# Kernel tuning notes

Measured on AMD Instinct MI355X. Metric: run time of the kernel, lower is better.

Reference implementation:

```python
import jax, jax.numpy as jnp
import numpy as np

B, CIN, N, E = 8192, 16, 96, 768
NF, EMB, NCLS = 64, 128, 210


def _p(key, shape, scale=0.05):
    return jax.random.normal(key, shape, dtype=jnp.float32) * scale


def setup_inputs() -> dict:
    key = jax.random.key(0)
    ks = jax.random.split(key, 20)
    return {
        "src": jax.random.normal(ks[0], (B, CIN, N), dtype=jnp.float32),
        "edge_index": jax.random.randint(ks[1], (2, E), 0, N, dtype=jnp.int32),
        "gcn1_w": _p(ks[2], (CIN, 64)), "gcn1_b": _p(ks[3], (64,)),
        "gcn2_w": _p(ks[4], (64, 32)), "gcn2_b": _p(ks[5], (32,)),
        "conv1_w": _p(ks[6], (NF, 32, 7)), "conv1_b": _p(ks[7], (NF,)),
        "conv2_w": _p(ks[8], (NF * 2, NF, 5)), "conv2_b": _p(ks[9], (NF * 2,)),
        "conv3_w": _p(ks[10], (NF * 4, NF * 2, 3)), "conv3_b": _p(ks[11], (NF * 4,)),
        "fc1_w": _p(ks[12], (3072, EMB)), "fc1_b": _p(ks[13], (EMB,)),
        "cls1_w": _p(ks[14], (EMB, EMB)), "cls1_b": _p(ks[15], (EMB,)),
        "cls2_w": _p(ks[16], (EMB, NCLS)), "cls2_b": _p(ks[17], (NCLS,)),
    }


def gcn_conv(x, edge_index, W, b):
    n = x.shape[1]
    loops = jnp.arange(n, dtype=edge_index.dtype)
    row = jnp.concatenate([edge_index[0], loops])  # targets
    col = jnp.concatenate([edge_index[1], loops])  # sources
    deg = jnp.zeros((n,), x.dtype).at[row].add(1.0)
    dinv = jax.lax.rsqrt(jnp.maximum(deg, 1e-12))
    norm = dinv[row] * dinv[col]                 # [E+N]
    h = x @ W                                    # [B, N, Fout]
    msgs = h[:, col, :] * norm[None, :, None]    # gather along node dim
    out = jnp.zeros_like(h).at[:, row, :].add(msgs)  # scatter-add
    return out + b


def conv1d(x, w, b, stride, pad):
    # x: [B, C, L], w: [O, C, K]
    y = jax.lax.conv_general_dilated(x, w, (stride,), [(pad, pad)],
                                     dimension_numbers=("NCH", "OIH", "NCH"))
    return y + b[None, :, None]


def reference(src, edge_index, gcn1_w, gcn1_b, gcn2_w, gcn2_b,
              conv1_w, conv1_b, conv2_w, conv2_b, conv3_w, conv3_b,
              fc1_w, fc1_b, cls1_w, cls1_b, cls2_w, cls2_b):
    x = jnp.transpose(src, (0, 2, 1))            # [B, N, CIN]
    x = jax.nn.relu(gcn_conv(x, edge_index, gcn1_w, gcn1_b))
    x = jax.nn.relu(gcn_conv(x, edge_index, gcn2_w, gcn2_b))
    x = jnp.transpose(x, (0, 2, 1))              # [B, 32, N]
    x = jax.nn.relu(conv1d(x, conv1_w, conv1_b, 2, 3))
    x = jax.nn.relu(conv1d(x, conv2_w, conv2_b, 2, 2))
    x = jax.nn.relu(conv1d(x, conv3_w, conv3_b, 2, 1))
    x = x.reshape(x.shape[0], -1)                # [B, 3072]
    feat = x @ fc1_w + fc1_b
    x = jax.nn.relu(feat)
    x = jax.nn.relu(x @ cls1_w + cls1_b)
    x = x @ cls2_w + cls2_b
    return (x, feat)
```

## Files before the change

### kernel.cpp

```cpp
#include <hip/hip_runtime.h>


typedef __attribute__((ext_vector_type(8))) short short8v;
typedef __attribute__((ext_vector_type(4))) float floatx4;

#define N_NODE 96
#define E_TOT  864
#define BATCH  8192ull

#define R0_OFF   0ull
#define R1_OFF   25165824ull
#define FR_OFF   50331648ull
#define R2_OFF   51380224ull
#define WT_OFF   52428800ull
#define W1N_OFF  (WT_OFF + 0)
#define W2N_OFF  (WT_OFF + 2048)
#define WC1_OFF  (WT_OFF + 4096)
#define WC2_OFF  (WT_OFF + 18432)
#define WC3_OFF  (WT_OFF + 59392)
#define WF1_OFF  (WT_OFF + 157696)
#define WL1_OFF  (WT_OFF + 550912)
#define WL2_OFF  (WT_OFF + 567296)
#define AH_OFF   (WT_OFF + 600064)

__device__ __forceinline__ unsigned short f2b(float f) {
    unsigned int u = __builtin_bit_cast(unsigned int, f);
    u += 0x7fffu + ((u >> 16) & 1u);
    return (unsigned short)(u >> 16);
}
__device__ __forceinline__ float b2f(unsigned short h) {
    unsigned int u = ((unsigned int)h) << 16;
    return __builtin_bit_cast(float, u);
}

__global__ void prep_all(const int* __restrict__ eidx,
                         const float* __restrict__ g1w, const float* __restrict__ g2w,
                         const float* __restrict__ w1, const float* __restrict__ w2,
                         const float* __restrict__ w3, const float* __restrict__ f1,
                         const float* __restrict__ l1, const float* __restrict__ l2,
                         unsigned short* __restrict__ wt,
                         unsigned short* __restrict__ ahf) {
    __shared__ int rowv[E_TOT];
    __shared__ int colv[E_TOT];
    __shared__ int degi[N_NODE];
    __shared__ float dinv[N_NODE];
    __shared__ float ad[96 * 96];
    const int tid = threadIdx.x;
    if (blockIdx.x == 0) {
        for (int e = tid; e < E_TOT; e += 256) {
            int r, c;
            if (e < 768) { r = eidx[e]; c = eidx[768 + e]; }
            else         { r = e - 768; c = r; }
            rowv[e] = r; colv[e] = c;
        }
        for (int n = tid; n < N_NODE; n += 256) degi[n] = 0;
        for (int i = tid; i < 9216; i += 256) ad[i] = 0.f;
        __syncthreads();
        for (int e = tid; e < E_TOT; e += 256) atomicAdd(&degi[rowv[e]], 1);
        __syncthreads();
        for (int n = tid; n < N_NODE; n += 256)
            dinv[n] = rsqrtf(fmaxf((float)degi[n], 1e-12f));
        __syncthreads();
        for (int e = tid; e < E_TOT; e += 256)
            atomicAdd(&ad[rowv[e] * 96 + colv[e]], dinv[rowv[e]] * dinv[colv[e]]);
        __syncthreads();
        for (int i = tid; i < 9216; i += 256) {
            int f = i >> 9, rm = i & 511;
            int ln = rm >> 3, j = rm & 7;
            int fm = f / 3, kk = f % 3;
            int row = fm * 16 + (ln & 15);
            int col = kk * 32 + (ln >> 4) * 8 + j;
            ahf[i] = f2b(ad[row * 96 + col]);
        }
        return;
    }
    long idx = (long)(blockIdx.x - 1) * 256 + tid;
    if (idx >= 600064) return;
    float v;
    if (idx < 2048) {
        int o = idx >> 5, c = idx & 31;
        v = (c < 16) ? g1w[c * 64 + o] : 0.f;
    } else if (idx < 4096) {
        long j = idx - 2048; int g = j >> 6, c = j & 63;
        v = g2w[c * 32 + g];
    } else {
        long base, KS;
        int region;
        if      (idx < 18432)  { base = 4096;   KS = 7;  region = 0; }
        else if (idx < 59392)  { base = 18432;  KS = 10; region = 1; }
        else if (idx < 157696) { base = 59392;  KS = 12; region = 2; }
        else if (idx < 550912) { base = 157696; KS = 96; region = 3; }
        else if (idx < 567296) { base = 550912; KS = 4;  region = 4; }
        else                   { base = 567296; KS = 4;  region = 5; }
        long local = idx - base;
        long g  = local / (KS * 512);
        long rm = local % (KS * 512);
        long ks = rm / 512;
        int lane = (int)((rm % 512) / 8);
        int j    = (int)(rm % 8);
        int quad = lane >> 4, n16 = lane & 15;
        int n = (int)(g * 16 + n16);
        int k = (int)(ks * 32 + quad * 8 + j);
        switch (region) {
            case 0: { int t = k / 32,  c = k % 32;  v = w1[n * 224 + c * 7 + t]; } break;
            case 1: { int t = k / 64,  c = k % 64;  v = w2[n * 320 + c * 5 + t]; } break;
            case 2: { int t = k / 128, c = k % 128; v = w3[n * 384 + c * 3 + t]; } break;
            case 3: { int t = k / 256, o = k % 256; v = f1[(o * 12 + t) * 128 + n]; } break;
            case 4: v = l1[k * 128 + n]; break;
            default: v = (n < 210) ? l2[k * 210 + n] : 0.f; break;
        }
    }
    wt[idx] = f2b(v);
}

__launch_bounds__(256, 4)
__global__ void gcn_fused(const float* __restrict__ src,
                          const unsigned short* __restrict__ ahf,
                          const unsigned short* __restrict__ w1n,
                          const unsigned short* __restrict__ w2n,
                          const float* __restrict__ b1,
                          const float* __restrict__ b2,
                          unsigned short* __restrict__ h2) {
    __shared__ __align__(16) unsigned short pool[4 * 4864];
    const int tid = threadIdx.x;
    const int w = tid >> 6, lane = tid & 63, quad = lane >> 4, m16 = lane & 15;
    unsigned short* P   = pool + w * 4864;
    unsigned short* XAc = P;
    unsigned short* H1W = P + 384;
    unsigned short* HWT = P + 1536;
    unsigned short* Cw  = P;
    const size_t bb = (size_t)blockIdx.x * 4 + w;

    short8v w1f[4], w2f[2][2];
    float bv1[4], bv2[2];
#pragma unroll
    for (int fn = 0; fn < 4; fn++) {
        w1f[fn] = *(const short8v*)&w1n[(fn * 16 + m16) * 32 + quad * 8];
        bv1[fn] = b1[fn * 16 + m16];
    }
#pragma unroll
    for (int fn = 0; fn < 2; fn++) {
#pragma unroll
        for (int kk = 0; kk < 2; kk++)
            w2f[fn][kk] = *(const short8v*)&w2n[(fn * 16 + m16) * 64 + kk * 32 + quad * 8];
        bv2[fn] = b2[fn * 16 + m16];
    }

    floatx4 acc[6] = {};
    const float* sB = src + bb * 1536 + (size_t)m16 * 96;
#pragma unroll
    for (int kk = 0; kk < 3; kk++) {
        float4 f0 = *(const float4*)&sB[kk * 32 + quad * 8];
        float4 f1 = *(const float4*)&sB[kk * 32 + quad * 8 + 4];
        short8v bfr;
        bfr[0] = (short)f2b(f0.x); bfr[1] = (short)f2b(f0.y);
        bfr[2] = (short)f2b(f0.z); bfr[3] = (short)f2b(f0.w);
        bfr[4] = (short)f2b(f1.x); bfr[5] = (short)f2b(f1.y);
        bfr[6] = (short)f2b(f1.z); bfr[7] = (short)f2b(f1.w);
#pragma unroll
        for (int fm = 0; fm < 6; fm++) {
            short8v afr = *(const short8v*)&ahf[((fm * 3 + kk) << 9) + lane * 8];
            acc[fm] = __builtin_amdgcn_mfma_f32_16x16x32_bf16(afr, bfr, acc[fm], 0, 0, 0);
        }
    }

#pragma unroll
    for (int cc = 0; cc < 6; cc++) {
#pragma unroll
        for (int r = 0; r < 4; r++)
            XAc[(quad * 4 + r) * 24 + m16] = f2b(acc[cc][r]);
        short8v afr1 = *(const short8v*)&XAc[m16 * 24 + quad * 8];
        floatx4 a1[4];
#pragma unroll
        for (int fn = 0; fn < 4; fn++) {
            floatx4 zc = {0.f, 0.f, 0.f, 0.f};
            a1[fn] = __builtin_amdgcn_mfma_f32_16x16x32_bf16(afr1, w1f[fn], zc, 0, 0, 0);
        }
#pragma unroll
        for (int fn = 0; fn < 4; fn++)
#pragma unroll
            for (int r = 0; r < 4; r++)
                H1W[(quad * 4 + r) * 72 + fn * 16 + m16] =
                    f2b(fmaxf(a1[fn][r] + bv1[fn], 0.f));
        floatx4 a2[2] = {};
#pragma unroll
        for (int kk = 0; kk < 2; kk++) {
            short8v afr2 = *(const short8v*)&H1W[m16 * 72 + kk * 32 + quad * 8];
#pragma unroll
            for (int fn = 0; fn < 2; fn++)
                a2[fn] = __builtin_amdgcn_mfma_f32_16x16x32_bf16(afr2, w2f[fn][kk], a2[fn], 0, 0, 0);
        }
#pragma unroll
        for (int fn = 0; fn < 2; fn++)
#pragma unroll
            for (int r = 0; r < 4; r++)
                HWT[(fn * 16 + m16) * 104 + cc * 16 + quad * 4 + r] = f2b(a2[fn][r]);
    }

    floatx4 c2a[6][2] = {};
#pragma unroll
    for (int kk = 0; kk < 3; kk++) {
        short8v bfr[2];
#pragma unroll
        for (int fn = 0; fn < 2; fn++)
            bfr[fn] = *(const short8v*)&HWT[(fn * 16 + m16) * 104 + kk * 32 + quad * 8];
#pragma unroll
        for (int fm = 0; fm < 6; fm++) {
            short8v afr = *(const short8v*)&ahf[((fm * 3 + kk) << 9) + lane * 8];
#pragma unroll
            for (int fn = 0; fn < 2; fn++)
                c2a[fm][fn] = __builtin_amdgcn_mfma_f32_16x16x32_bf16(afr, bfr[fn], c2a[fm][fn], 0, 0, 0);
        }
    }
#pragma unroll
    for (int fm = 0; fm < 6; fm++)
#pragma unroll
        for (int fn = 0; fn < 2; fn++)
#pragma unroll
            for (int r = 0; r < 4; r++)
                Cw[(fm * 16 + quad * 4 + r) * 32 + fn * 16 + m16] =
                    f2b(fmaxf(c2a[fm][fn][r] + bv2[fn], 0.f));
#pragma unroll
    for (int it = 0; it < 6; it++) {
        int idx = it * 64 + lane;
        int node = idx >> 2, q8 = idx & 3;
        *(uint4*)&h2[((size_t)node * BATCH + bb) * 32 + q8 * 8] =
            *(const uint4*)&Cw[idx * 8];
    }
}

template<int WM, int FN, int NTAP, int CIN, int NOUT, int STRIDE, int PAD, int LIN, int BK, int MODE>
__launch_bounds__(256)
__global__ void gemm_slab(const unsigned short* __restrict__ in,
                          const unsigned short* __restrict__ wn,
                          const float* __restrict__ bias,
                          unsigned short* __restrict__ outb,
                          float* __restrict__ outf) {
    constexpr int BM  = WM * 32;
    constexpr int BN  = FN * 32;
    constexpr int BKP = BK + 8;
    constexpr int CPT = CIN / BK;
    constexpr int NC  = NTAP * CPT;
    constexpr int KS  = NTAP * CIN / 32;
    constexpr int NV  = BM * BK / 8 / 256;
    constexpr int RPV = 256 / (BK / 8);
    constexpr int SZ1 = 2 * BM * BKP;
    constexpr int SZ2 = (MODE == 4) ? 16 : BM * (BN + 8);
    constexpr int POOL = SZ1 > SZ2 ? SZ1 : SZ2;
    __shared__ __align__(16) unsigned short pool[POOL];
    const int tid = threadIdx.x;
    const size_t b0 = blockIdx.x * BM;
    const int n0 = blockIdx.y * BN;
    const int l  = blockIdx.z;
    const int w = tid >> 6, lane = tid & 63, quad = lane >> 4, m16 = lane & 15;
    const int wm = w >> 1, wq = w & 1;
    const int mbase = wm * (WM * 16), nbase = wq * (FN * 16);
    const int gw = (n0 + nbase) >> 4;
    const int lr = tid / (BK / 8);
    const int lc = tid % (BK / 8);
    floatx4 acc[WM][FN] = {};
    const short8v zz8 = {0, 0, 0, 0, 0, 0, 0, 0};

    short8v pre[NV], nxt[NV];
    {
        int pos = STRIDE * l - PAD;
        if (pos >= 0 && pos < LIN) {
            const unsigned short* ag = in + ((size_t)pos * BATCH + b0) * CIN;
#pragma unroll
            for (int v = 0; v < NV; v++)
                pre[v] = *(const short8v*)&ag[(size_t)(lr + v * RPV) * CIN + lc * 8];
        } else {
#pragma unroll
            for (int v = 0; v < NV; v++) pre[v] = zz8;
        }
#pragma unroll
        for (int v = 0; v < NV; v++)
            *(short8v*)&pool[(lr + v * RPV) * BKP + lc * 8] = pre[v];
    }
    int p = 0;
#pragma unroll
    for (int ch = 0; ch < NC; ++ch) {
        __syncthreads();
        if (ch + 1 < NC) {
            int t = (ch + 1) / CPT, inner = (ch + 1) % CPT;
            int pos = STRIDE * l + t - PAD;
            if (pos >= 0 && pos < LIN) {
                const unsigned short* ag = in + ((size_t)pos * BATCH + b0) * CIN + inner * BK;
#pragma unroll
                for (int v = 0; v < NV; v++)
                    nxt[v] = *(const short8v*)&ag[(size_t)(lr + v * RPV) * CIN + lc * 8];
            } else {
#pragma unroll
                for (int v = 0; v < NV; v++) nxt[v] = zz8;
            }
        }
        const unsigned short* As = pool + p * BM * BKP;
        const int kbase = (ch / CPT) * CIN + (ch % CPT) * BK;
#pragma unroll
        for (int kk = 0; kk < BK; kk += 32) {
            const int ksG = (kbase + kk) >> 5;
            short8v bfr[FN];
#pragma unroll
            for (int fn = 0; fn < FN; fn++)
                bfr[fn] = *(const short8v*)&wn[(((size_t)(gw + fn) * KS + ksG) << 9) + lane * 8];
#pragma unroll
            for (int fm = 0; fm < WM; fm++) {
                short8v afr = *(const short8v*)&As[(mbase + fm * 16 + m16) * BKP + kk + quad * 8];
#pragma unroll
                for (int fn = 0; fn < FN; fn++)
                    acc[fm][fn] = __builtin_amdgcn_mfma_f32_16x16x32_bf16(afr, bfr[fn], acc[fm][fn], 0, 0, 0);
            }
        }
        if (ch + 1 < NC) {
            unsigned short* Ad = pool + (p ^ 1) * BM * BKP;
#pragma unroll
            for (int v = 0; v < NV; v++)
                *(short8v*)&Ad[(lr + v * RPV) * BKP + lc * 8] = nxt[v];
        }
        p ^= 1;
    }

    if constexpr (MODE == 4) {
#pragma unroll
        for (int fn = 0; fn < FN; fn++) {
            int cg = n0 + nbase + fn * 16 + m16;
            float bv = (cg < 210) ? bias[cg] : 0.f;
            if (cg < 210) {
#pragma unroll
                for (int fm = 0; fm < WM; fm++)
#pragma unroll
                    for (int r = 0; r < 4; r++) {
                        size_t row = b0 + mbase + fm * 16 + quad * 4 + r;
                        outf[row * 210 + cg] = acc[fm][fn][r] + bv;
                    }
            }
        }
    } else {
        float bv[FN];
#pragma unroll
        for (int fn = 0; fn < FN; fn++) bv[fn] = bias[n0 + nbase + fn * 16 + m16];
        __syncthreads();
        unsigned short* Cs = pool;
#pragma unroll
        for (int fm = 0; fm < WM; fm++)
#pragma unroll
            for (int r = 0; r < 4; r++) {
                int row = mbase + fm * 16 + quad * 4 + r;
#pragma unroll
                for (int fn = 0; fn < FN; fn++)
                    Cs[row * (BN + 8) + nbase + fn * 16 + m16] =
                        f2b(fmaxf(acc[fm][fn][r] + bv[fn], 0.f));
            }
        __syncthreads();
        for (int u = tid; u < BM * (BN / 8); u += 256) {
            int r = u / (BN / 8), cc = u % (BN / 8);
            *(short8v*)&outb[((size_t)l * BATCH + b0 + r) * NOUT + n0 + cc * 8] =
                *(short8v*)&Cs[r * (BN + 8) + cc * 8];
        }
    }
}

__launch_bounds__(256)
__global__ void fc1_splitk(const unsigned short* __restrict__ c3,
                           const unsigned short* __restrict__ wf1,
                           float* __restrict__ part) {
    __shared__ __align__(16) unsigned short pool[2 * 128 * 72];
    const int tid = threadIdx.x;
    const size_t b0 = blockIdx.x * 128;
    const int kg = blockIdx.z;
    const int w = tid >> 6, lane = tid & 63, quad = lane >> 4, m16 = lane & 15;
    const int wm = w >> 1, wq = w & 1;
    const int mbase = wm * 64, nbase = wq * 64;
    const int gw = nbase >> 4;
    const int lr = tid >> 3, lc = tid & 7;
    floatx4 acc[4][4] = {};
    short8v pre[4], nxt[4];

    {
        const unsigned short* ag = c3 + ((size_t)(kg * 2) * BATCH + b0) * 256;
#pragma unroll
        for (int v = 0; v < 4; v++)
            pre[v] = *(const short8v*)&ag[(size_t)(lr + v * 32) * 256 + lc * 8];
#pragma unroll
        for (int v = 0; v < 4; v++)
            *(short8v*)&pool[(lr + v * 32) * 72 + lc * 8] = pre[v];
    }
    int p = 0;
#pragma unroll
    for (int s = 0; s < 8; ++s) {
        __syncthreads();
        if (s + 1 < 8) {
            int t = kg * 2 + ((s + 1) >> 2), inner = (s + 1) & 3;
            const unsigned short* ag = c3 + ((size_t)t * BATCH + b0) * 256 + inner * 64;
#pragma unroll
            for (int v = 0; v < 4; v++)
                nxt[v] = *(const short8v*)&ag[(size_t)(lr + v * 32) * 256 + lc * 8];
        }
        const unsigned short* As = pool + p * 128 * 72;
        const int kbase = (kg * 2 + (s >> 2)) * 256 + (s & 3) * 64;
#pragma unroll
        for (int kk = 0; kk < 64; kk += 32) {
            const int ksG = (kbase + kk) >> 5;
            short8v bfr[4];
#pragma unroll
            for (int fn = 0; fn < 4; fn++)
                bfr[fn] = *(const short8v*)&wf1[(((size_t)(gw + fn) * 96 + ksG) << 9) + lane * 8];
#pragma unroll
            for (int fm = 0; fm < 4; fm++) {
                short8v afr = *(const short8v*)&As[(mbase + fm * 16 + m16) * 72 + kk + quad * 8];
#pragma unroll
                for (int fn = 0; fn < 4; fn++)
                    acc[fm][fn] = __builtin_amdgcn_mfma_f32_16x16x32_bf16(afr, bfr[fn], acc[fm][fn], 0, 0, 0);
            }
        }
        if (s + 1 < 8) {
            unsigned short* Ad = pool + (p ^ 1) * 128 * 72;
#pragma unroll
            for (int v = 0; v < 4; v++)
                *(short8v*)&Ad[(lr + v * 32) * 72 + lc * 8] = nxt[v];
        }
        p ^= 1;
    }
    float* pg = part + (size_t)kg * BATCH * 128;
#pragma unroll
    for (int fm = 0; fm < 4; fm++)
#pragma unroll
        for (int r = 0; r < 4; r++) {
            size_t row = b0 + mbase + fm * 16 + quad * 4 + r;
#pragma unroll
            for (int fn = 0; fn < 4; fn++)
                pg[row * 128 + nbase + fn * 16 + m16] = acc[fm][fn][r];
        }
}

__launch_bounds__(256)
__global__ void fc1_reduce(const float* __restrict__ part, const float* __restrict__ bias,
                           float* __restrict__ feat, unsigned short* __restrict__ fr) {
    const size_t idx = (size_t)blockIdx.x * 256 + threadIdx.x;
    const size_t row = idx >> 5;
    const int    c4  = (int)(idx & 31);
    float4 s = *(const float4*)&bias[c4 * 4];
#pragma unroll
    for (int z = 0; z < 6; z++) {
        float4 p = *(const float4*)&part[(z * BATCH + row) * 128 + c4 * 4];
        s.x += p.x; s.y += p.y; s.z += p.z; s.w += p.w;
    }
    *(float4*)&feat[row * 128 + c4 * 4] = s;
    unsigned int d0 = (unsigned int)f2b(fmaxf(s.x, 0.f)) |
                      ((unsigned int)f2b(fmaxf(s.y, 0.f)) << 16);
    unsigned int d1 = (unsigned int)f2b(fmaxf(s.z, 0.f)) |
                      ((unsigned int)f2b(fmaxf(s.w, 0.f)) << 16);
    *(uint2*)&fr[row * 128 + c4 * 4] = make_uint2(d0, d1);
}

extern "C" void kernel_launch(void* const* d_in, const int* in_sizes, int n_in,
                              void* d_out, int out_size, void* d_ws, size_t ws_size,
                              hipStream_t stream) {
    const float* src  = (const float*)d_in[0];
    const int*   eidx = (const int*)  d_in[1];
    const float* g1w  = (const float*)d_in[2];
    const float* g1b  = (const float*)d_in[3];
    const float* g2w  = (const float*)d_in[4];
    const float* g2b  = (const float*)d_in[5];
    const float* cv1w = (const float*)d_in[6];
    const float* cv1b = (const float*)d_in[7];
    const float* cv2w = (const float*)d_in[8];
    const float* cv2b = (const float*)d_in[9];
    const float* cv3w = (const float*)d_in[10];
    const float* cv3b = (const float*)d_in[11];
    const float* fc1w = (const float*)d_in[12];
    const float* fc1b = (const float*)d_in[13];
    const float* cl1w = (const float*)d_in[14];
    const float* cl1b = (const float*)d_in[15];
    const float* cl2w = (const float*)d_in[16];
    const float* cl2b = (const float*)d_in[17];

    unsigned short* ws16 = (unsigned short*)d_ws;
    float* wsF = (float*)d_ws;
    float* out = (float*)d_out;

    unsigned short* h2  = ws16 + R0_OFF;
    unsigned short* c1  = ws16 + R1_OFF;
    unsigned short* c2  = ws16 + R0_OFF;
    unsigned short* c3  = ws16 + R1_OFF;
    float*          part = wsF;
    unsigned short* fr  = ws16 + FR_OFF;
    unsigned short* r2  = ws16 + R2_OFF;
    unsigned short* w1n = ws16 + W1N_OFF;
    unsigned short* w2n = ws16 + W2N_OFF;
    unsigned short* wc1 = ws16 + WC1_OFF;
    unsigned short* wc2 = ws16 + WC2_OFF;
    unsigned short* wc3 = ws16 + WC3_OFF;
    unsigned short* wf1 = ws16 + WF1_OFF;
    unsigned short* wl1 = ws16 + WL1_OFF;
    unsigned short* wl2 = ws16 + WL2_OFF;
    unsigned short* ahf = ws16 + AH_OFF;

    float* feat_out = out + 8192ull * 210ull;

    prep_all<<<2346, 256, 0, stream>>>(eidx, g1w, g2w, cv1w, cv2w, cv3w, fc1w, cl1w, cl2w,
                                       ws16 + WT_OFF, ahf);
    gcn_fused<<<2048, 256, 0, stream>>>(src, ahf, w1n, w2n, g1b, g2b, h2);
    gemm_slab<8, 2, 7, 32, 64, 2, 3, 96, 32, 0>
        <<<dim3(32, 1, 48), 256, 0, stream>>>(h2, wc1, cv1b, c1, nullptr);
    gemm_slab<4, 4, 5, 64, 128, 2, 2, 48, 64, 0>
        <<<dim3(64, 1, 24), 256, 0, stream>>>(c1, wc2, cv2b, c2, nullptr);
    gemm_slab<4, 4, 3, 128, 256, 2, 1, 24, 64, 0>
        <<<dim3(64, 2, 12), 256, 0, stream>>>(c2, wc3, cv3b, c3, nullptr);
    fc1_splitk<<<dim3(64, 1, 6), 256, 0, stream>>>(c3, wf1, part);
    fc1_reduce<<<1024, 256, 0, stream>>>(part, fc1b, feat_out, fr);
    gemm_slab<2, 2, 1, 128, 128, 1, 0, 1, 64, 0>
        <<<dim3(128, 2, 1), 256, 0, stream>>>(fr, wl1, cl1b, r2, nullptr);
    gemm_slab<2, 2, 1, 128, 256, 1, 0, 1, 64, 4>
        <<<dim3(128, 4, 1), 256, 0, stream>>>(r2, wl2, cl2b, nullptr, out);
}
```

Measured before the change: 274.5 us.

## Add split-bf16 GCN precision and replace conv GEMMs with sliding-window ring kernel

The GCN adjacency and input are split into bf16 hi/lo parts and extra MFMAs are issued to recover near-fp32 accuracy. Adjacency accumulation now runs as a deterministic per-row loop instead of atomics. The three conv1d layers move from gemm_slab to a new conv_ring kernel. It keeps a shared-memory ring of input time slabs so each loaded slab is reused across overlapping output positions, and prefetches the next two slabs into registers. This cuts redundant input loads, but it adds 3x or 2x MFMAs in the GCN, reads weights directly from global memory, and uses far fewer, larger blocks.

```diff
diff --git a/kernel.cpp b/kernel.cpp
--- a/kernel.cpp
+++ b/kernel.cpp
@@ -61,8 +61,12 @@
         for (int n = tid; n < N_NODE; n += 256)
             dinv[n] = rsqrtf(fmaxf((float)degi[n], 1e-12f));
         __syncthreads();
-        for (int e = tid; e < E_TOT; e += 256)
-            atomicAdd(&ad[rowv[e] * 96 + colv[e]], dinv[rowv[e]] * dinv[colv[e]]);
+        if (tid < N_NODE) {
+            float dr = dinv[tid];
+            float* adr = &ad[tid * 96];
+            for (int e = 0; e < E_TOT; e++)
+                if (rowv[e] == tid) adr[colv[e]] += dr * dinv[colv[e]];
+        }
         __syncthreads();
         for (int i = tid; i < 9216; i += 256) {
             int f = i >> 9, rm = i & 511;
@@ -70,7 +74,10 @@
             int fm = f / 3, kk = f % 3;
             int row = fm * 16 + (ln & 15);
             int col = kk * 32 + (ln >> 4) * 8 + j;
-            ahf[i] = f2b(ad[row * 96 + col]);
+            float a = ad[row * 96 + col];
+            unsigned short hi = f2b(a);
+            ahf[i] = hi;
+            ahf[9216 + i] = f2b(a - b2f(hi));
         }
         return;
     }
@@ -131,6 +138,8 @@
     unsigned short* Cw  = P;
     const size_t bb = (size_t)blockIdx.x * 4 + w;
 
+    *(unsigned int*)&XAc[(lane >> 2) * 24 + 16 + (lane & 3) * 2] = 0;
+
     short8v w1f[4], w2f[2][2];
     float bv1[4], bv2[2];
 #pragma unroll
@@ -152,15 +161,21 @@
     for (int kk = 0; kk < 3; kk++) {
         float4 f0 = *(const float4*)&sB[kk * 32 + quad * 8];
         float4 f1 = *(const float4*)&sB[kk * 32 + quad * 8 + 4];
-        short8v bfr;
-        bfr[0] = (short)f2b(f0.x); bfr[1] = (short)f2b(f0.y);
-        bfr[2] = (short)f2b(f0.z); bfr[3] = (short)f2b(f0.w);
-        bfr[4] = (short)f2b(f1.x); bfr[5] = (short)f2b(f1.y);
-        bfr[6] = (short)f2b(f1.z); bfr[7] = (short)f2b(f1.w);
+        float fv[8] = {f0.x, f0.y, f0.z, f0.w, f1.x, f1.y, f1.z, f1.w};
+        short8v bh, bl;
+#pragma unroll
+        for (int j = 0; j < 8; j++) {
+            unsigned short hi = f2b(fv[j]);
+            bh[j] = (short)hi;
+            bl[j] = (short)f2b(fv[j] - b2f(hi));
+        }
 #pragma unroll
         for (int fm = 0; fm < 6; fm++) {
-            short8v afr = *(const short8v*)&ahf[((fm * 3 + kk) << 9) + lane * 8];
-            acc[fm] = __builtin_amdgcn_mfma_f32_16x16x32_bf16(afr, bfr, acc[fm], 0, 0, 0);
+            short8v ah = *(const short8v*)&ahf[((fm * 3 + kk) << 9) + lane * 8];
+            short8v al = *(const short8v*)&ahf[9216 + ((fm * 3 + kk) << 9) + lane * 8];
+            acc[fm] = __builtin_amdgcn_mfma_f32_16x16x32_bf16(ah, bh, acc[fm], 0, 0, 0);
+            acc[fm] = __builtin_amdgcn_mfma_f32_16x16x32_bf16(al, bh, acc[fm], 0, 0, 0);
+            acc[fm] = __builtin_amdgcn_mfma_f32_16x16x32_bf16(ah, bl, acc[fm], 0, 0, 0);
         }
     }
 
@@ -206,10 +221,13 @@
             bfr[fn] = *(const short8v*)&HWT[(fn * 16 + m16) * 104 + kk * 32 + quad * 8];
 #pragma unroll
         for (int fm = 0; fm < 6; fm++) {
-            short8v afr = *(const short8v*)&ahf[((fm * 3 + kk) << 9) + lane * 8];
-#pragma unroll
-            for (int fn = 0; fn < 2; fn++)
-                c2a[fm][fn] = __builtin_amdgcn_mfma_f32_16x16x32_bf16(afr, bfr[fn], c2a[fm][fn], 0, 0, 0);
+            short8v ah = *(const short8v*)&ahf[((fm * 3 + kk) << 9) + lane * 8];
+            short8v al = *(const short8v*)&ahf[9216 + ((fm * 3 + kk) << 9) + lane * 8];
+#pragma unroll
+            for (int fn = 0; fn < 2; fn++) {
+                c2a[fm][fn] = __builtin_amdgcn_mfma_f32_16x16x32_bf16(ah, bfr[fn], c2a[fm][fn], 0, 0, 0);
+                c2a[fm][fn] = __builtin_amdgcn_mfma_f32_16x16x32_bf16(al, bfr[fn], c2a[fm][fn], 0, 0, 0);
+            }
         }
     }
 #pragma unroll
@@ -226,6 +244,125 @@
         int node = idx >> 2, q8 = idx & 3;
         *(uint4*)&h2[((size_t)node * BATCH + bb) * 32 + q8 * 8] =
             *(const uint4*)&Cw[idx * 8];
+    }
+}
+
+template<int NTAP, int CIN, int NOUT, int PAD, int LIN, int ZLEN>
+__launch_bounds__(256, 2)
+__global__ void conv_ring(const unsigned short* __restrict__ in,
+                          const unsigned short* __restrict__ wn,
+                          const float* __restrict__ bias,
+                          unsigned short* __restrict__ outb) {
+    constexpr int R    = (NTAP + 1 <= 4) ? 4 : 8;
+    constexpr int BM   = 64;
+    constexpr int BKP  = CIN + 8;
+    constexpr int SLAB = BM * BKP;
+    constexpr int CPT  = CIN / 32;
+    constexpr int KS   = NTAP * CPT;
+    constexpr int FN   = NOUT / 32;
+    constexpr int NV   = BM * CIN / 8 / 256;
+    constexpr int RPV  = 256 / (CIN / 8);
+    __shared__ __align__(16) unsigned short ring[R * SLAB];
+    const int tid = threadIdx.x;
+    const size_t b0 = (size_t)blockIdx.x * BM;
+    const int z0 = blockIdx.z * ZLEN;
+    const int lane = tid & 63, quad = lane >> 4, m16 = lane & 15;
+    const int w = tid >> 6, wm = w >> 1, wq = w & 1;
+    const int mbase = wm * 32, nbase = wq * (FN * 16);
+    const int gw = nbase >> 4;
+    const int lr = tid / (CIN / 8), lc = tid % (CIN / 8);
+    const short8v zz8 = {0, 0, 0, 0, 0, 0, 0, 0};
+
+    float bv[FN];
+#pragma unroll
+    for (int fn = 0; fn < FN; fn++) bv[fn] = bias[nbase + fn * 16 + m16];
+
+    const int T0 = 2 * z0 - PAD;
+#pragma unroll
+    for (int i = 0; i < NTAP; i++) {
+        int t = T0 + i;
+        short8v v[NV];
+        if (t >= 0 && t < LIN) {
+            const unsigned short* ag = in + ((size_t)t * BATCH + b0) * CIN;
+#pragma unroll
+            for (int vv = 0; vv < NV; vv++)
+                v[vv] = *(const short8v*)&ag[(size_t)(lr + vv * RPV) * CIN + lc * 8];
+        } else {
+#pragma unroll
+            for (int vv = 0; vv < NV; vv++) v[vv] = zz8;
+        }
+        unsigned short* S = ring + (t & (R - 1)) * SLAB;
+#pragma unroll
+        for (int vv = 0; vv < NV; vv++)
+            *(short8v*)&S[(lr + vv * RPV) * BKP + lc * 8] = v[vv];
+    }
+
+    for (int zl = 0; zl < ZLEN; zl++) {
+        const int T = 2 * (z0 + zl) - PAD;
+        __syncthreads();
+        short8v nx0[NV], nx1[NV];
+        if (zl + 1 < ZLEN) {
+            int ta = T + NTAP, tb = T + NTAP + 1;
+            if (ta >= 0 && ta < LIN) {
+                const unsigned short* ag = in + ((size_t)ta * BATCH + b0) * CIN;
+#pragma unroll
+                for (int vv = 0; vv < NV; vv++)
+                    nx0[vv] = *(const short8v*)&ag[(size_t)(lr + vv * RPV) * CIN + lc * 8];
+            } else {
+#pragma unroll
+                for (int vv = 0; vv < NV; vv++) nx0[vv] = zz8;
+            }
+            if (tb >= 0 && tb < LIN) {
+                const unsigned short* ag = in + ((size_t)tb * BATCH + b0) * CIN;
+#pragma unroll
+                for (int vv = 0; vv < NV; vv++)
+                    nx1[vv] = *(const short8v*)&ag[(size_t)(lr + vv * RPV) * CIN + lc * 8];
+            } else {
+#pragma unroll
+                for (int vv = 0; vv < NV; vv++) nx1[vv] = zz8;
+            }
+        }
+        floatx4 acc[2][FN] = {};
+#pragma unroll
+        for (int i = 0; i < NTAP; i++) {
+            const unsigned short* S = ring + ((T + i) & (R - 1)) * SLAB;
+#pragma unroll
+            for (int kk = 0; kk < CPT; kk++) {
+                const int ksG = i * CPT + kk;
+                short8v bfr[FN];
+#pragma unroll
+                for (int fn = 0; fn < FN; fn++)
+                    bfr[fn] = *(const short8v*)&wn[(((size_t)(gw + fn) * KS + ksG) << 9) + lane * 8];
+#pragma unroll
+                for (int fm = 0; fm < 2; fm++) {
+                    short8v afr = *(const short8v*)&S[(mbase + fm * 16 + m16) * BKP + kk * 32 + quad * 8];
+#pragma unroll
+                    for (int fn = 0; fn < FN; fn++)
+                        acc[fm][fn] = __builtin_amdgcn_mfma_f32_16x16x32_bf16(afr, bfr[fn], acc[fm][fn], 0, 0, 0);
+                }
+            }
+        }
+        const size_t zb = (size_t)(z0 + zl) * BATCH + b0;
+#pragma unroll
+        for (int fm = 0; fm < 2; fm++)
+#pragma unroll
+            for (int r = 0; r < 4; r++) {
+                const size_t rowo = (zb + mbase + fm * 16 + quad * 4 + r) * NOUT;
+#pragma unroll
+                for (int fn = 0; fn < FN; fn++)
+                    outb[rowo + nbase + fn * 16 + m16] =
+                        f2b(fmaxf(acc[fm][fn][r] + bv[fn], 0.f));
+            }
+        __syncthreads();
+        if (zl + 1 < ZLEN) {
+            unsigned short* Sa = ring + ((T + NTAP) & (R - 1)) * SLAB;
+            unsigned short* Sb = ring + ((T + NTAP + 1) & (R - 1)) * SLAB;
+#pragma unroll
+            for (int vv = 0; vv < NV; vv++) {
+                *(short8v*)&Sa[(lr + vv * RPV) * BKP + lc * 8] = nx0[vv];
+                *(short8v*)&Sb[(lr + vv * RPV) * BKP + lc * 8] = nx1[vv];
+            }
+        }
     }
 }
 
@@ -501,12 +638,12 @@
     prep_all<<<2346, 256, 0, stream>>>(eidx, g1w, g2w, cv1w, cv2w, cv3w, fc1w, cl1w, cl2w,
                                        ws16 + WT_OFF, ahf);
     gcn_fused<<<2048, 256, 0, stream>>>(src, ahf, w1n, w2n, g1b, g2b, h2);
-    gemm_slab<8, 2, 7, 32, 64, 2, 3, 96, 32, 0>
-        <<<dim3(32, 1, 48), 256, 0, stream>>>(h2, wc1, cv1b, c1, nullptr);
-    gemm_slab<4, 4, 5, 64, 128, 2, 2, 48, 64, 0>
-        <<<dim3(64, 1, 24), 256, 0, stream>>>(c1, wc2, cv2b, c2, nullptr);
-    gemm_slab<4, 4, 3, 128, 256, 2, 1, 24, 64, 0>
-        <<<dim3(64, 2, 12), 256, 0, stream>>>(c2, wc3, cv3b, c3, nullptr);
+    conv_ring<7, 32, 64, 3, 96, 12>
+        <<<dim3(128, 1, 4), 256, 0, stream>>>(h2, wc1, cv1b, c1);
+    conv_ring<5, 64, 128, 2, 48, 6>
+        <<<dim3(128, 1, 4), 256, 0, stream>>>(c1, wc2, cv2b, c2);
+    conv_ring<3, 128, 256, 1, 24, 3>
+        <<<dim3(128, 1, 4), 256, 0, stream>>>(c2, wc3, cv3b, c3);
     fc1_splitk<<<dim3(64, 1, 6), 256, 0, stream>>>(c3, wf1, part);
     fc1_reduce<<<1024, 256, 0, stream>>>(part, fc1b, feat_out, fr);
     gemm_slab<2, 2, 1, 128, 128, 1, 0, 1, 64, 0>
```

New measurement: 448.5 us. 1.63x slower.
